# Optimization experiments

Measured on AMD Instinct MI355X. Metric: run time of the kernel, lower is better.

The kernel has to match this reference:

```python
import jax, jax.numpy as jnp
import numpy as np

N_NODES = 50000
N_EDGES = 600000
D_IN = 128
D_OUT = 128


def mean_propagate(x, edge_index, num_nodes):
    # edge_index[0] = source nodes, edge_index[1] = destination nodes
    src, dst = edge_index[0], edge_index[1]
    gathered = x[src]                                   # [E, D]
    summed = jax.ops.segment_sum(gathered, dst, num_segments=num_nodes)  # [N, D]
    deg = jax.ops.segment_sum(jnp.ones((edge_index.shape[1],), dtype=x.dtype), dst,
                              num_segments=num_nodes)   # [N]
    deg = jnp.maximum(deg, 1.0)
    return summed / deg[:, None]


def setup_inputs() -> dict:
    key = jax.random.key(0)
    k1, k2, k3 = jax.random.split(key, 3)
    x = jax.random.normal(k1, (N_NODES, D_IN), dtype=jnp.float32)
    edge_index = jax.random.randint(k2, (2, N_EDGES), 0, N_NODES, dtype=jnp.int64)
    # nn.Linear(in_channels*3, out_channels): weight [out, 3*in], bias [out]
    W = jax.random.normal(k3, (D_OUT, 3 * D_IN), dtype=jnp.float32) / np.sqrt(3 * D_IN)
    b = jnp.zeros((D_OUT,), dtype=jnp.float32)
    return {"x": x, "edge_index": edge_index, "W": W, "b": b}


def reference(x, edge_index, W, b):
    n = x.shape[0]
    hop1 = mean_propagate(x, edge_index, n)
    hop2 = mean_propagate(hop1, edge_index, n)
    feats = jnp.concatenate([x, hop1, hop2], axis=-1)   # [N, 3*D]
    return feats @ W.T + b                              # [N, D_OUT]
```

## Files before the change

### kernel.cpp

```cpp
#include <hip/hip_runtime.h>

#define N_NODES 50000
#define N_EDGES 600000
#define D 128
#define K3 (3 * D)
#define NB_G 1563
#define NB_H 2344
#define NREP 8

typedef __attribute__((ext_vector_type(8))) short short8;
typedef __attribute__((ext_vector_type(4))) float floatx4;
typedef __attribute__((ext_vector_type(8))) unsigned short ushort8;

static __device__ __forceinline__ unsigned short f2bf(float f) {
    unsigned u = __float_as_uint(f);
    u += 0x7fff + ((u >> 16) & 1);
    return (unsigned short)(u >> 16);
}
static __device__ __forceinline__ float bf2f(unsigned short s) {
    return __uint_as_float(((unsigned)s) << 16);
}
static __device__ __forceinline__ unsigned pack2(float a, float b) {
    return (unsigned)f2bf(a) | ((unsigned)f2bf(b) << 16);
}

__global__ __launch_bounds__(256) void prep_kernel(const float* __restrict__ x,
                                                   const float* __restrict__ W,
                                                   unsigned short* __restrict__ xb,
                                                   unsigned short* __restrict__ Wr,
                                                   int* __restrict__ counts8) {
    const int stride = gridDim.x * 256;
    const int t0 = blockIdx.x * 256 + threadIdx.x;
    for (int i = t0; i < NREP * N_NODES; i += stride) counts8[i] = 0;
    for (unsigned t = t0; t < (unsigned)N_NODES * 16; t += stride) {
        unsigned n = t >> 4;
        unsigned c = (t & 15u) << 3;
        const float4 v0 = *(const float4*)(x + (size_t)n * D + c);
        const float4 v1 = *(const float4*)(x + (size_t)n * D + c + 4);
        ushort8 o;
        o[0] = f2bf(v0.x); o[1] = f2bf(v0.y); o[2] = f2bf(v0.z); o[3] = f2bf(v0.w);
        o[4] = f2bf(v1.x); o[5] = f2bf(v1.y); o[6] = f2bf(v1.z); o[7] = f2bf(v1.w);
        *(ushort8*)(xb + (size_t)n * D + c) = o;
    }
    for (unsigned id = t0; id < 24u * 4u * 64u; id += stride) {
        unsigned T = id >> 8;
        unsigned ks = (id >> 6) & 3u;
        unsigned lane = id & 63u;
        unsigned c = lane & 15u;
        unsigned q = lane >> 4;
        unsigned row = (T & 7u) * 16u + c;
        unsigned k = (T >> 3) * 128u + ks * 32u + q * 8u;
        const float4 v0 = *(const float4*)(W + (size_t)row * K3 + k);
        const float4 v1 = *(const float4*)(W + (size_t)row * K3 + k + 4);
        ushort8 o;
        o[0] = f2bf(v0.x); o[1] = f2bf(v0.y); o[2] = f2bf(v0.z); o[3] = f2bf(v0.w);
        o[4] = f2bf(v1.x); o[5] = f2bf(v1.y); o[6] = f2bf(v1.z); o[7] = f2bf(v1.w);
        *(ushort8*)(Wr + (size_t)id * 8) = o;
    }
}

#define LDSROW 104
__global__ __launch_bounds__(256) void gemmhist_kernel(const unsigned short* __restrict__ xb,
                                                       const unsigned short* __restrict__ Wr,
                                                       const float* __restrict__ bias,
                                                       const int* __restrict__ dst,
                                                       unsigned short* __restrict__ z,
                                                       int* __restrict__ counts8) {
    __shared__ unsigned short lds[4 * 32 * LDSROW];
    const int blk = blockIdx.x;
    if (blk >= NB_G) {
        int hb = blk - NB_G;
        int e = hb * 256 + threadIdx.x;
        if (e < N_EDGES) atomicAdd(&counts8[(hb & 7) * N_NODES + dst[e]], 1);
        return;
    }
    const int tid = threadIdx.x;
    const int wave = tid >> 6;
    const int lane = tid & 63;
    const int col = lane & 15;
    const int quad = lane >> 4;
    const int mbase = blk * 32;
    const int T0 = wave * 6;

    int r0 = mbase + col;
    int r1 = mbase + 16 + col;
    if (r0 >= N_NODES) r0 = N_NODES - 1;
    if (r1 >= N_NODES) r1 = N_NODES - 1;
    const unsigned short* ap0 = xb + (size_t)r0 * D + quad * 8;
    const unsigned short* ap1 = xb + (size_t)r1 * D + quad * 8;

    floatx4 acc0[6], acc1[6];
#pragma unroll
    for (int t = 0; t < 6; ++t) {
        acc0[t] = (floatx4){0.f, 0.f, 0.f, 0.f};
        acc1[t] = (floatx4){0.f, 0.f, 0.f, 0.f};
    }

#pragma unroll
    for (int ks = 0; ks < 4; ++ks) {
        short8 a0 = *(const short8*)(ap0 + ks * 32);
        short8 a1 = *(const short8*)(ap1 + ks * 32);
#pragma unroll
        for (int t = 0; t < 6; ++t) {
            short8 bb = *(const short8*)(Wr + (size_t)(((T0 + t) * 4 + ks) * 64 + lane) * 8);
            acc0[t] = __builtin_amdgcn_mfma_f32_16x16x32_bf16(bb, a0, acc0[t], 0, 0, 0);
            acc1[t] = __builtin_amdgcn_mfma_f32_16x16x32_bf16(bb, a1, acc1[t], 0, 0, 0);
        }
    }

    unsigned short* wlds = lds + wave * 32 * LDSROW;
#pragma unroll
    for (int t = 0; t < 6; ++t) {
        int T = T0 + t;
        float4 bq = (float4){0.f, 0.f, 0.f, 0.f};
        if (T < 8) bq = *(const float4*)(bias + T * 16 + quad * 4);
        uint2 p;
        p.x = pack2(acc0[t][0] + bq.x, acc0[t][1] + bq.y);
        p.y = pack2(acc0[t][2] + bq.z, acc0[t][3] + bq.w);
        *(uint2*)(wlds + col * LDSROW + t * 16 + quad * 4) = p;
        uint2 q2;
        q2.x = pack2(acc1[t][0] + bq.x, acc1[t][1] + bq.y);
        q2.y = pack2(acc1[t][2] + bq.z, acc1[t][3] + bq.w);
        *(uint2*)(wlds + (col + 16) * LDSROW + t * 16 + quad * 4) = q2;
    }
    __syncthreads();
#pragma unroll
    for (int it = 0; it < 6; ++it) {
        int id = it * 64 + lane;
        int row = id / 12;
        int ch = id - row * 12;
        int node = mbase + row;
        ushort8 v = *(const ushort8*)(wlds + row * LDSROW + ch * 8);
        if (node < N_NODES)
            *(ushort8*)(z + (size_t)node * K3 + T0 * 16 + ch * 8) = v;
    }
}

__global__ __launch_bounds__(256) void bsum_kernel(const int* __restrict__ counts8,
                                                   int* __restrict__ ctot,
                                                   int* __restrict__ bsum) {
    __shared__ int wsum[4];
    int tid = threadIdx.x;
    int i = blockIdx.x * 256 + tid;
    int v = 0;
    if (i < N_NODES) {
#pragma unroll
        for (int r = 0; r < NREP; ++r) v += counts8[r * N_NODES + i];
        ctot[i] = v;
    }
#pragma unroll
    for (int d = 32; d >= 1; d >>= 1) v += __shfl_xor(v, d);
    if ((tid & 63) == 0) wsum[tid >> 6] = v;
    __syncthreads();
    if (tid == 0) bsum[blockIdx.x] = wsum[0] + wsum[1] + wsum[2] + wsum[3];
}

__global__ __launch_bounds__(256) void scan_bsum_kernel(const int* __restrict__ bsum,
                                                        int* __restrict__ bexcl,
                                                        int* __restrict__ off, int nb) {
    __shared__ int wsum[4];
    int tid = threadIdx.x;
    int lane = tid & 63, wid = tid >> 6;
    int v = (tid < nb) ? bsum[tid] : 0;
    int x = v;
#pragma unroll
    for (int d = 1; d < 64; d <<= 1) {
        int u = __shfl_up(x, d);
        if (lane >= d) x += u;
    }
    if (lane == 63) wsum[wid] = x;
    __syncthreads();
    int prefix = 0;
    for (int w = 0; w < wid; ++w) prefix += wsum[w];
    if (tid < nb) bexcl[tid] = prefix + x - v;
    if (tid == 0) off[N_NODES] = N_EDGES;
}

__global__ __launch_bounds__(256) void scan_final_kernel(const int* __restrict__ ctot,
                                                         const int* __restrict__ counts8,
                                                         const int* __restrict__ bexcl,
                                                         int* __restrict__ off,
                                                         int* __restrict__ cursor8) {
    __shared__ int wsum[4];
    int tid = threadIdx.x;
    int lane = tid & 63, wid = tid >> 6;
    int i = blockIdx.x * 256 + tid;
    int v = (i < N_NODES) ? ctot[i] : 0;
    int x = v;
#pragma unroll
    for (int d = 1; d < 64; d <<= 1) {
        int u = __shfl_up(x, d);
        if (lane >= d) x += u;
    }
    if (lane == 63) wsum[wid] = x;
    __syncthreads();
    int prefix = 0;
    for (int w = 0; w < wid; ++w) prefix += wsum[w];
    if (i < N_NODES) {
        int excl = bexcl[blockIdx.x] + prefix + x - v;
        off[i] = excl;
        int run = excl;
#pragma unroll
        for (int r = 0; r < NREP; ++r) {
            cursor8[r * N_NODES + i] = run;
            run += counts8[r * N_NODES + i];
        }
    }
}

__global__ __launch_bounds__(256) void fill_kernel(const int* __restrict__ src,
                                                   const int* __restrict__ dst,
                                                   int* __restrict__ cursor8,
                                                   int* __restrict__ csr_src) {
    int e = blockIdx.x * blockDim.x + threadIdx.x;
    if (e < N_EDGES) {
        int r = blockIdx.x & 7;
        int pos = atomicAdd(&cursor8[r * N_NODES + dst[e]], 1);
        csr_src[pos] = src[e];
    }
}

__global__ __launch_bounds__(256) void gather1_kernel(const unsigned short* __restrict__ z,
                                                      const int* __restrict__ off,
                                                      const int* __restrict__ csr_src,
                                                      unsigned short* __restrict__ tb) {
    unsigned n = (blockIdx.x * 256 + threadIdx.x) >> 6;
    if (n >= N_NODES) return;
    const int lane = threadIdx.x & 63;
    const int s = lane >> 4;
    const unsigned c = (lane & 15u) << 3;
    const unsigned short* fin = z + 256 + c;
    const int2 ee = *(const int2*)(off + n);
    const int e0 = ee.x, e1 = ee.y;
    float acc[8] = {0.f, 0.f, 0.f, 0.f, 0.f, 0.f, 0.f, 0.f};
    for (int base = (e0 & ~3) + s * 4; base < e1; base += 16) {
        int4 idx = *(const int4*)(csr_src + base);
        float m0 = (base >= e0) ? 1.f : 0.f;
        float m1 = (base + 1 >= e0 && base + 1 < e1) ? 1.f : 0.f;
        float m2 = (base + 2 >= e0 && base + 2 < e1) ? 1.f : 0.f;
        float m3 = (base + 3 >= e0 && base + 3 < e1) ? 1.f : 0.f;
        int s0 = min(max(idx.x, 0), N_NODES - 1);
        int s1 = min(max(idx.y, 0), N_NODES - 1);
        int s2 = min(max(idx.z, 0), N_NODES - 1);
        int s3 = min(max(idx.w, 0), N_NODES - 1);
        ushort8 v0 = *(const ushort8*)(fin + (size_t)s0 * K3);
        ushort8 v1 = *(const ushort8*)(fin + (size_t)s1 * K3);
        ushort8 v2 = *(const ushort8*)(fin + (size_t)s2 * K3);
        ushort8 v3 = *(const ushort8*)(fin + (size_t)s3 * K3);
#pragma unroll
        for (int j = 0; j < 8; ++j)
            acc[j] += (m0 * bf2f(v0[j]) + m1 * bf2f(v1[j])) +
                      (m2 * bf2f(v2[j]) + m3 * bf2f(v3[j]));
    }
#pragma unroll
    for (int j = 0; j < 8; ++j) {
        acc[j] += __shfl_xor(acc[j], 16);
        acc[j] += __shfl_xor(acc[j], 32);
    }
    if (s == 0) {
        float inv = 1.0f / fmaxf((float)(e1 - e0), 1.0f);
        ushort8 za = *(const ushort8*)(z + (size_t)n * K3 + 128 + c);
        ushort8 o;
#pragma unroll
        for (int j = 0; j < 8; ++j) o[j] = f2bf(bf2f(za[j]) + acc[j] * inv);
        *(ushort8*)(tb + (size_t)n * D + c) = o;
    }
}

__global__ __launch_bounds__(256) void gather2_kernel(const unsigned short* __restrict__ z,
                                                      const unsigned short* __restrict__ tb,
                                                      const int* __restrict__ off,
                                                      const int* __restrict__ csr_src,
                                                      float* __restrict__ out) {
    unsigned n = (blockIdx.x * 256 + threadIdx.x) >> 6;
    if (n >= N_NODES) return;
    const int lane = threadIdx.x & 63;
    const int s = lane >> 4;
    const unsigned c = (lane & 15u) << 3;
    const unsigned short* fin = tb + c;
    const int2 ee = *(const int2*)(off + n);
    const int e0 = ee.x, e1 = ee.y;
    float acc[8] = {0.f, 0.f, 0.f, 0.f, 0.f, 0.f, 0.f, 0.f};
    for (int base = (e0 & ~3) + s * 4; base < e1; base += 16) {
        int4 idx = *(const int4*)(csr_src + base);
        float m0 = (base >= e0) ? 1.f : 0.f;
        float m1 = (base + 1 >= e0 && base + 1 < e1) ? 1.f : 0.f;
        float m2 = (base + 2 >= e0 && base + 2 < e1) ? 1.f : 0.f;
        float m3 = (base + 3 >= e0 && base + 3 < e1) ? 1.f : 0.f;
        int s0 = min(max(idx.x, 0), N_NODES - 1);
        int s1 = min(max(idx.y, 0), N_NODES - 1);
        int s2 = min(max(idx.z, 0), N_NODES - 1);
        int s3 = min(max(idx.w, 0), N_NODES - 1);
        ushort8 v0 = *(const ushort8*)(fin + (size_t)s0 * D);
        ushort8 v1 = *(const ushort8*)(fin + (size_t)s1 * D);
        ushort8 v2 = *(const ushort8*)(fin + (size_t)s2 * D);
        ushort8 v3 = *(const ushort8*)(fin + (size_t)s3 * D);
#pragma unroll
        for (int j = 0; j < 8; ++j)
            acc[j] += (m0 * bf2f(v0[j]) + m1 * bf2f(v1[j])) +
                      (m2 * bf2f(v2[j]) + m3 * bf2f(v3[j]));
    }
#pragma unroll
    for (int j = 0; j < 8; ++j) {
        acc[j] += __shfl_xor(acc[j], 16);
        acc[j] += __shfl_xor(acc[j], 32);
    }
    if (s == 0) {
        float inv = 1.0f / fmaxf((float)(e1 - e0), 1.0f);
        ushort8 za = *(const ushort8*)(z + (size_t)n * K3 + c);
        float4 q0, q1;
        q0.x = bf2f(za[0]) + acc[0] * inv;
        q0.y = bf2f(za[1]) + acc[1] * inv;
        q0.z = bf2f(za[2]) + acc[2] * inv;
        q0.w = bf2f(za[3]) + acc[3] * inv;
        q1.x = bf2f(za[4]) + acc[4] * inv;
        q1.y = bf2f(za[5]) + acc[5] * inv;
        q1.z = bf2f(za[6]) + acc[6] * inv;
        q1.w = bf2f(za[7]) + acc[7] * inv;
        *(float4*)(out + (size_t)n * D + c) = q0;
        *(float4*)(out + (size_t)n * D + c + 4) = q1;
    }
}

extern "C" void kernel_launch(void* const* d_in, const int* in_sizes, int n_in,
                              void* d_out, int out_size, void* d_ws, size_t ws_size,
                              hipStream_t stream) {
    const float* x = (const float*)d_in[0];
    const int* ei = (const int*)d_in[1];
    const float* W = (const float*)d_in[2];
    const float* b = (const float*)d_in[3];
    float* out = (float*)d_out;
    const int* src = ei;
    const int* dst = ei + N_EDGES;

    unsigned short* xb = (unsigned short*)d_ws;
    unsigned short* z = xb + (size_t)N_NODES * D;
    unsigned short* tb = z + (size_t)N_NODES * K3;
    unsigned short* Wr = tb + (size_t)N_NODES * D;
    int* counts8 = (int*)(Wr + 6144 * 8);
    int* ctot = counts8 + NREP * N_NODES;
    int* bsum = ctot + N_NODES;
    int* bexcl = bsum + 256;
    int* off = bexcl + 256;
    int* cursor8 = off + (N_NODES + 4);
    int* csr_src = cursor8 + NREP * N_NODES;

    const int NB = (N_NODES + 255) / 256;

    prep_kernel<<<800, 256, 0, stream>>>(x, W, xb, Wr, counts8);
    gemmhist_kernel<<<NB_G + NB_H, 256, 0, stream>>>(xb, Wr, b, dst, z, counts8);
    bsum_kernel<<<NB, 256, 0, stream>>>(counts8, ctot, bsum);
    scan_bsum_kernel<<<1, 256, 0, stream>>>(bsum, bexcl, off, NB);
    scan_final_kernel<<<NB, 256, 0, stream>>>(ctot, counts8, bexcl, off, cursor8);
    fill_kernel<<<(N_EDGES + 255) / 256, 256, 0, stream>>>(src, dst, cursor8, csr_src);

    const int ggrid = (N_NODES * 64 + 255) / 256;
    gather1_kernel<<<ggrid, 256, 0, stream>>>(z, off, csr_src, tb);
    gather2_kernel<<<ggrid, 256, 0, stream>>>(z, tb, off, csr_src, out);
}
```

Baseline: 206.8 us.

## Fuse three scan kernels into one cooperative grid-sync kernel; preload GEMM operands

```diff
diff --git a/kernel.cpp b/kernel.cpp
--- a/kernel.cpp
+++ b/kernel.cpp
@@ -1,4 +1,7 @@
 #include <hip/hip_runtime.h>
+#include <hip/hip_cooperative_groups.h>
+
+namespace cg = cooperative_groups;
 
 #define N_NODES 50000
 #define N_EDGES 600000
@@ -7,6 +10,8 @@
 #define NB_G 1563
 #define NB_H 2344
 #define NREP 8
+#define NB 196
+#define LDSROW 104
 
 typedef __attribute__((ext_vector_type(8))) short short8;
 typedef __attribute__((ext_vector_type(4))) float floatx4;
@@ -59,7 +64,6 @@
     }
 }
 
-#define LDSROW 104
 __global__ __launch_bounds__(256) void gemmhist_kernel(const unsigned short* __restrict__ xb,
                                                        const unsigned short* __restrict__ Wr,
                                                        const float* __restrict__ bias,
@@ -89,22 +93,31 @@
     const unsigned short* ap0 = xb + (size_t)r0 * D + quad * 8;
     const unsigned short* ap1 = xb + (size_t)r1 * D + quad * 8;
 
+    short8 a0r[4], a1r[4];
+#pragma unroll
+    for (int ks = 0; ks < 4; ++ks) {
+        a0r[ks] = *(const short8*)(ap0 + ks * 32);
+        a1r[ks] = *(const short8*)(ap1 + ks * 32);
+    }
+    short8 br[24];
+#pragma unroll
+    for (int t = 0; t < 6; ++t)
+#pragma unroll
+        for (int ks = 0; ks < 4; ++ks)
+            br[t * 4 + ks] = *(const short8*)(Wr + (size_t)(((T0 + t) * 4 + ks) * 64 + lane) * 8);
+
     floatx4 acc0[6], acc1[6];
 #pragma unroll
     for (int t = 0; t < 6; ++t) {
         acc0[t] = (floatx4){0.f, 0.f, 0.f, 0.f};
         acc1[t] = (floatx4){0.f, 0.f, 0.f, 0.f};
     }
-
 #pragma unroll
     for (int ks = 0; ks < 4; ++ks) {
-        short8 a0 = *(const short8*)(ap0 + ks * 32);
-        short8 a1 = *(const short8*)(ap1 + ks * 32);
 #pragma unroll
         for (int t = 0; t < 6; ++t) {
-            short8 bb = *(const short8*)(Wr + (size_t)(((T0 + t) * 4 + ks) * 64 + lane) * 8);
-            acc0[t] = __builtin_amdgcn_mfma_f32_16x16x32_bf16(bb, a0, acc0[t], 0, 0, 0);
-            acc1[t] = __builtin_amdgcn_mfma_f32_16x16x32_bf16(bb, a1, acc1[t], 0, 0, 0);
+            acc0[t] = __builtin_amdgcn_mfma_f32_16x16x32_bf16(br[t * 4 + ks], a0r[ks], acc0[t], 0, 0, 0);
+            acc1[t] = __builtin_amdgcn_mfma_f32_16x16x32_bf16(br[t * 4 + ks], a1r[ks], acc1[t], 0, 0, 0);
         }
     }
 
@@ -133,6 +146,72 @@
         ushort8 v = *(const ushort8*)(wlds + row * LDSROW + ch * 8);
         if (node < N_NODES)
             *(ushort8*)(z + (size_t)node * K3 + T0 * 16 + ch * 8) = v;
+    }
+}
+
+__global__ __launch_bounds__(256) void coopscan_kernel(const int* __restrict__ counts8,
+                                                       int* __restrict__ ctot,
+                                                       int* __restrict__ bsum,
+                                                       int* __restrict__ bexcl,
+                                                       int* __restrict__ off,
+                                                       int* __restrict__ cursor8) {
+    cg::grid_group grid = cg::this_grid();
+    __shared__ int wsum[4];
+    const int tid = threadIdx.x;
+    const int lane = tid & 63;
+    const int wid = tid >> 6;
+    const int i = blockIdx.x * 256 + tid;
+
+    int v = 0;
+    if (i < N_NODES) {
+#pragma unroll
+        for (int r = 0; r < NREP; ++r) v += counts8[r * N_NODES + i];
+        ctot[i] = v;
+    }
+    int rv = v;
+#pragma unroll
+    for (int d = 32; d >= 1; d >>= 1) rv += __shfl_xor(rv, d);
+    if (lane == 0) wsum[wid] = rv;
+    __syncthreads();
+    if (tid == 0) bsum[blockIdx.x] = wsum[0] + wsum[1] + wsum[2] + wsum[3];
+    grid.sync();
+
+    if (blockIdx.x == 0) {
+        int b = (tid < NB) ? bsum[tid] : 0;
+        int xs = b;
+#pragma unroll
+        for (int d = 1; d < 64; d <<= 1) {
+            int u = __shfl_up(xs, d);
+            if (lane >= d) xs += u;
+        }
+        if (lane == 63) wsum[wid] = xs;
+        __syncthreads();
+        int prefix = 0;
+        for (int w = 0; w < wid; ++w) prefix += wsum[w];
+        if (tid < NB) bexcl[tid] = prefix + xs - b;
+        if (tid == 0) off[N_NODES] = N_EDGES;
+    }
+    grid.sync();
+
+    int xs = v;
+#pragma unroll
+    for (int d = 1; d < 64; d <<= 1) {
+        int u = __shfl_up(xs, d);
+        if (lane >= d) xs += u;
+    }
+    if (lane == 63) wsum[wid] = xs;
+    __syncthreads();
+    int prefix = 0;
+    for (int w = 0; w < wid; ++w) prefix += wsum[w];
+    if (i < N_NODES) {
+        int excl = bexcl[blockIdx.x] + prefix + xs - v;
+        off[i] = excl;
+        int run = excl;
+#pragma unroll
+        for (int r = 0; r < NREP; ++r) {
+            cursor8[r * N_NODES + i] = run;
+            run += counts8[r * N_NODES + i];
+        }
     }
 }
 
@@ -339,22 +418,31 @@
     unsigned short* Wr = tb + (size_t)N_NODES * D;
     int* counts8 = (int*)(Wr + 6144 * 8);
     int* ctot = counts8 + NREP * N_NODES;
-    int* bsum = ctot + N_NODES;
-    int* bexcl = bsum + 256;
-    int* off = bexcl + 256;
-    int* cursor8 = off + (N_NODES + 4);
-    int* csr_src = cursor8 + NREP * N_NODES;
-
-    const int NB = (N_NODES + 255) / 256;
+    int* bsumv = ctot + N_NODES;
+    int* bexclv = bsumv + 256;
+    int* offv = bexclv + 256;
+    int* cursor8v = offv + (N_NODES + 4);
+    int* csrv = cursor8v + NREP * N_NODES;
 
     prep_kernel<<<800, 256, 0, stream>>>(x, W, xb, Wr, counts8);
     gemmhist_kernel<<<NB_G + NB_H, 256, 0, stream>>>(xb, Wr, b, dst, z, counts8);
-    bsum_kernel<<<NB, 256, 0, stream>>>(counts8, ctot, bsum);
-    scan_bsum_kernel<<<1, 256, 0, stream>>>(bsum, bexcl, off, NB);
-    scan_final_kernel<<<NB, 256, 0, stream>>>(ctot, counts8, bexcl, off, cursor8);
-    fill_kernel<<<(N_EDGES + 255) / 256, 256, 0, stream>>>(src, dst, cursor8, csr_src);
+
+    {
+        const int* c8 = counts8;
+        void* kargs[] = {(void*)&c8,    (void*)&ctot,  (void*)&bsumv,
+                         (void*)&bexclv, (void*)&offv, (void*)&cursor8v};
+        hipError_t err = hipLaunchCooperativeKernel((void*)coopscan_kernel, dim3(NB),
+                                                    dim3(256), kargs, 0, stream);
+        if (err != hipSuccess) {
+            bsum_kernel<<<NB, 256, 0, stream>>>(counts8, ctot, bsumv);
+            scan_bsum_kernel<<<1, 256, 0, stream>>>(bsumv, bexclv, offv, NB);
+            scan_final_kernel<<<NB, 256, 0, stream>>>(ctot, counts8, bexclv, offv, cursor8v);
+        }
+    }
+
+    fill_kernel<<<(N_EDGES + 255) / 256, 256, 0, stream>>>(src, dst, cursor8v, csrv);
 
     const int ggrid = (N_NODES * 64 + 255) / 256;
-    gather1_kernel<<<ggrid, 256, 0, stream>>>(z, off, csr_src, tb);
-    gather2_kernel<<<ggrid, 256, 0, stream>>>(z, tb, off, csr_src, out);
-}
+    gather1_kernel<<<ggrid, 256, 0, stream>>>(z, offv, csrv, tb);
+    gather2_kernel<<<ggrid, 256, 0, stream>>>(z, tb, offv, csrv, out);
+}
```

After: 255.5 us. +23.5%, slower.
